# Kernel optimization log

Hardware: AMD Instinct MI355X
Metric: run time of the kernel (lower is better)

Reference implementation:

```python
import jax, jax.numpy as jnp
import numpy as np

T = 8          # num_timesteps
H = 8          # num_heads
D = 128        # lifting_dim
ROPE_BASE = 10000.0


def apply_time_only_rope(x, num_nodes, num_timesteps, base=ROPE_BASE):
    # x: [B, H, num_nodes*num_timesteps, d_head], time-major flattening
    B, Hh, S, dh = x.shape
    half = dh // 2
    times = jnp.arange(num_timesteps, dtype=jnp.float32)
    freqs = 1.0 / base ** (2.0 * jnp.arange(half, dtype=jnp.float32) / dh)
    angle = times[:, None] * freqs[None, :]                 # [T, half]
    positions = jnp.repeat(jnp.arange(num_timesteps), num_nodes)  # [S]
    cos_g = jnp.cos(angle)[positions]                       # [S, half]
    sin_g = jnp.sin(angle)[positions]
    t1 = x[..., 0::2]
    t2 = x[..., 1::2]
    r0 = t1 * cos_g - t2 * sin_g
    r1 = t1 * sin_g + t2 * cos_g
    return jnp.stack([r0, r1], axis=-1).reshape(x.shape)


def setup_inputs() -> dict:
    key = jax.random.key(0)
    ks = jax.random.split(key, 16)
    B_T, N, E = 32, 2048, 8192
    inp = {
        'x_0': jax.random.normal(ks[0], (B_T, N, D), jnp.float32),
        'edge_attr': jax.random.normal(ks[1], (B_T, E, D), jnp.float32),
        'q_data': jax.random.normal(ks[2], (B_T, N, D), jnp.float32),
    }
    def lin(k):
        kw, kb = jax.random.split(k)
        return (jax.random.normal(kw, (D, D), jnp.float32) * 0.02,
                jax.random.normal(kb, (D,), jnp.float32) * 0.02)
    inp['Wq'], inp['bq'] = lin(ks[3])
    inp['Wk0'], inp['bk0'] = lin(ks[4])
    inp['Wv0'], inp['bv0'] = lin(ks[5])
    inp['Wk1'], inp['bk1'] = lin(ks[6])
    inp['Wv1'], inp['bv1'] = lin(ks[7])
    inp['Wo'], inp['bo'] = lin(ks[8])
    return inp


def reference(x_0, edge_attr, q_data, Wq, bq, Wk0, bk0, Wv0, bv0, Wk1, bk1, Wv1, bv1, Wo, bo):
    B_T, N, d = x_0.shape
    B = B_T // T
    dh = d // H

    def flatten_st(a):  # [B*T, M, d] -> [B, T*M, d]
        return a.reshape(B, T * a.shape[1], d)

    qf = flatten_st(q_data) @ Wq.T + bq                     # [B, T*N, d]
    q = qf.reshape(B, H, N * T, dh)                         # faithful torch .view
    q = jax.nn.softmax(q, axis=-1)
    q = apply_time_only_rope(q, N, T)

    out = q
    for (feat, Wk, bk, Wv, bv) in ((x_0, Wk0, bk0, Wv0, bv0),
                                   (edge_attr, Wk1, bk1, Wv1, bv1)):
        M = feat.shape[1]
        hf = flatten_st(feat)                               # [B, T*M, d]
        k = (hf @ Wk.T + bk).reshape(B, H, M * T, dh)
        v = (hf @ Wv.T + bv).reshape(B, H, M * T, dh)
        k = apply_time_only_rope(k, M, T)
        k = jax.nn.softmax(k, axis=-1)
        k_cumsum = k.sum(axis=-2, keepdims=True)            # [B,H,1,dh]
        D_inv = 1.0 / jnp.maximum((q * k_cumsum).sum(axis=-1, keepdims=True), 1e-8)
        kv = jnp.einsum('bhsd,bhse->bhde', k, v)            # [B,H,dh,dh]
        out = q + jnp.einsum('bhsd,bhde->bhse', q, kv) * D_inv

    out = out.transpose(0, 2, 1, 3).reshape(B, N * T, d)
    out = out @ Wo.T + bo
    return out.reshape(B * T, N, d)                         # unflatten_spatiotemporal
```

## Files before the change

### kernel.cpp

```cpp
#include <hip/hip_runtime.h>
#include <hip/hip_bf16.h>
#include <math.h>


typedef __attribute__((ext_vector_type(8))) short short8;
typedef __attribute__((ext_vector_type(4))) float float4v;

#define LN1E4_OVER8 1.1512925464970229f

#define OFF_QWS   0
#define OFF_FRG_Q 4194304
#define OFF_FRG_O 4202496
#define OFF_BFRG  4210688
#define OFF_KV    4227072
#define OFF_KCS   4235264
#define OFF_PART  4235776

__device__ __forceinline__ unsigned short f2bf(float f) {
    __hip_bfloat16 h = __float2bfloat16(f);
    return *reinterpret_cast<unsigned short*>(&h);
}
__device__ __forceinline__ float bf2f(unsigned short s) {
    return __uint_as_float(((unsigned)s) << 16);
}
__device__ __forceinline__ unsigned pk2(float a, float b) {
    __hip_bfloat162 h = __float22bfloat162_rn(make_float2(a, b));
    return *reinterpret_cast<unsigned*>(&h);
}
template<int C> __device__ __forceinline__ float dppadd(float x) {
    int r = __builtin_amdgcn_update_dpp(0, __float_as_int(x), C, 0xF, 0xF, true);
    return x + __int_as_float(r);
}
__device__ __forceinline__ float sum16(float x) {
    x = dppadd<0xB1>(x);
    x = dppadd<0x4E>(x);
    x = dppadd<0x141>(x);
    x = dppadd<0x140>(x);
    return x;
}
__device__ __forceinline__ float qperm1(float x) {
    int r = __builtin_amdgcn_update_dpp(0, __float_as_int(x), 0xB1, 0xF, 0xF, true);
    return __int_as_float(r);
}

__global__ void k_prep(const float* __restrict__ Wq, const float* __restrict__ Wk1,
                       const float* __restrict__ Wv1, const float* __restrict__ Wo,
                       float* __restrict__ ws) {
    int i = blockIdx.x * 256 + threadIdx.x;
    if (i < 32768) {
        int j = i & 16383;
        int jE = j & 7, lane = (j >> 3) & 63, km = (j >> 9) & 3, cg = j >> 11;
        int n = cg * 16 + (lane & 15);
        int kk = km * 32 + (lane >> 4) * 8 + jE;
        const float* W = (i < 16384) ? Wq : Wo;
        unsigned short* dst = (unsigned short*)(ws + ((i < 16384) ? OFF_FRG_Q : OFF_FRG_O));
        dst[j] = f2bf(W[n * 128 + kk]);
    } else {
        int j = i - 32768;
        int jE = j & 7, lane = (j >> 3) & 63, km = (j >> 9) & 3, cg = j >> 11;
        int n = cg * 16 + (lane & 15);
        int k = km * 32 + (lane >> 4) * 8 + jE;
        float w = (cg < 8) ? Wk1[n * 128 + k] : Wv1[(n - 128) * 128 + k];
        ((unsigned short*)(ws + OFF_BFRG))[j] = f2bf(w);
    }
}

__global__ __launch_bounds__(256, 2) void k_q(const float* __restrict__ qd,
                                              const float* __restrict__ bq,
                                              float* __restrict__ ws) {
    __shared__ __align__(16) unsigned short aT[128 * 128];
    unsigned* qws32 = (unsigned*)(ws + OFF_QWS);
    int t = threadIdx.x, blk = blockIdx.x;
    int wave = t >> 6, lane = t & 63, quad = lane >> 4, n = lane & 15;
    long base = (long)blk * 128;
    int b = blk >> 7;
    int h = (blk & 127) >> 4;
    int s0 = (blk & 15) * 1024;
    int t1 = (blk & 15) >> 1;

    const short8* fq = (const short8*)((const unsigned short*)(ws + OFF_FRG_Q));
    short8 Bf[2][4];
    #pragma unroll
    for (int ct = 0; ct < 2; ++ct)
        #pragma unroll
        for (int km = 0; km < 4; ++km)
            Bf[ct][km] = fq[((2 * wave + ct) * 4 + km) * 64 + lane];

    #pragma unroll
    for (int i = 0; i < 16; ++i) {
        int idx = i * 256 + t;
        int row = idx >> 5, c4 = idx & 31;
        float4 v = ((const float4*)qd)[(base + row) * 32 + c4];
        unsigned short* p = aT + row * 128 + (((c4 >> 1) ^ (row & 7)) << 3) + (c4 & 1) * 4;
        *(uint2*)p = make_uint2(pk2(v.x, v.y), pk2(v.z, v.w));
    }
    __syncthreads();

    float4v acc[8][2];
    #pragma unroll
    for (int rt = 0; rt < 8; ++rt)
        #pragma unroll
        for (int ct = 0; ct < 2; ++ct) acc[rt][ct] = (float4v){0.f, 0.f, 0.f, 0.f};

    #pragma unroll
    for (int rt = 0; rt < 8; ++rt) {
        int row = rt * 16 + n;
        #pragma unroll
        for (int km = 0; km < 4; ++km) {
            short8 Af = *(const short8*)(aT + row * 128 + (((km * 4 + quad) ^ (n & 7)) << 3));
            acc[rt][0] = __builtin_amdgcn_mfma_f32_16x16x32_bf16(Af, Bf[0][km], acc[rt][0], 0, 0, 0);
            acc[rt][1] = __builtin_amdgcn_mfma_f32_16x16x32_bf16(Af, Bf[1][km], acc[rt][1], 0, 0, 0);
        }
    }

    float fr = __expf(-LN1E4_OVER8 * (float)(n >> 1));
    float sa, ca; __sincosf((float)t1 * fr, &sa, &ca);
    float sgn = (n & 1) ? sa : -sa;

    #pragma unroll
    for (int rt = 0; rt < 8; ++rt)
        #pragma unroll
        for (int ct = 0; ct < 2; ++ct) {
            int cg = 2 * wave + ct;
            float bias = bq[cg * 16 + n];
            float4v x = acc[rt][ct];
            #pragma unroll
            for (int i = 0; i < 4; ++i) {
                float e = __expf(x[i] + bias);
                float s = sum16(e);
                float q = e / s;
                float r = fmaf(qperm1(q), sgn, q * ca);
                unsigned pkd = ((unsigned)f2bf(qperm1(r)) << 16) | (unsigned)f2bf(r);
                if ((n & 1) == 0) {
                    int sp = s0 + (rt * 16 + quad * 4 + i) * 8 + cg;
                    long qoff = ((long)(b * 8 + h) * 16384 + sp) * 16 + n;
                    qws32[qoff >> 1] = pkd;
                }
            }
        }
}

__global__ __launch_bounds__(256, 3) void k_kv(const float* __restrict__ ea,
                                               const float* __restrict__ bk,
                                               const float* __restrict__ bv,
                                               float* __restrict__ ws) {
    __shared__ __align__(16) char smem[49152];
    unsigned short* aT = (unsigned short*)smem;

    int t = threadIdx.x, blk = blockIdx.x;
    int wave = t >> 6, lane = t & 63, quad = lane >> 4, n = lane & 15;
    unsigned short* kbuf = (unsigned short*)(smem + 32768) + wave * 2048;
    unsigned short* vbuf = kbuf + 1024;
    long base = (long)blk * 128;
    int sl = (blk & 511) << 7;
    int t2 = (sl & 8191) >> 10;

    #pragma unroll
    for (int i = 0; i < 16; ++i) {
        int idx = i * 256 + t;
        int row = idx >> 5, c4 = idx & 31;
        float4 v = ((const float4*)ea)[(base + row) * 32 + c4];
        unsigned short* p = aT + row * 128 + (((c4 >> 1) ^ (row & 7)) << 3) + (c4 & 1) * 4;
        *(uint2*)p = make_uint2(pk2(v.x, v.y), pk2(v.z, v.w));
    }

    const short8* bfrag = (const short8*)((const unsigned short*)(ws + OFF_BFRG));
    short8 Bf[4][4];
    #pragma unroll
    for (int ct = 0; ct < 4; ++ct) {
        int cg = (ct < 2) ? (2 * wave + ct) : (8 + 2 * wave + (ct - 2));
        #pragma unroll
        for (int km = 0; km < 4; ++km)
            Bf[ct][km] = bfrag[(cg * 4 + km) * 64 + lane];
    }

    float bias[4];
    #pragma unroll
    for (int ct = 0; ct < 4; ++ct)
        bias[ct] = (ct < 2) ? bk[(2 * wave + ct) * 16 + n] : bv[(2 * wave + ct - 2) * 16 + n];
    float fr = __expf(-LN1E4_OVER8 * (float)(n >> 1));
    float sv, cvv; __sincosf((float)t2 * fr, &sv, &cvv);
    float sgn = (n & 1) ? sv : -sv;
    float kcsacc = 0.f;
    float4v kvacc = (float4v){0.f, 0.f, 0.f, 0.f};

    __syncthreads();

    #pragma unroll
    for (int pair = 0; pair < 4; ++pair) {
        float4v acc[2][4];
        #pragma unroll
        for (int rtl = 0; rtl < 2; ++rtl)
            #pragma unroll
            for (int ct = 0; ct < 4; ++ct) acc[rtl][ct] = (float4v){0.f, 0.f, 0.f, 0.f};

        #pragma unroll
        for (int rtl = 0; rtl < 2; ++rtl) {
            int row = (pair * 2 + rtl) * 16 + n;
            short8 Af[4];
            #pragma unroll
            for (int km = 0; km < 4; ++km)
                Af[km] = *(const short8*)(aT + row * 128 + (((km * 4 + quad) ^ (n & 7)) << 3));
            #pragma unroll
            for (int ct = 0; ct < 4; ++ct)
                #pragma unroll
                for (int km = 0; km < 4; ++km)
                    acc[rtl][ct] = __builtin_amdgcn_mfma_f32_16x16x32_bf16(Af[km], Bf[ct][km], acc[rtl][ct], 0, 0, 0);
        }

        #pragma unroll
        for (int rtl = 0; rtl < 2; ++rtl)
            #pragma unroll
            for (int ct = 0; ct < 4; ++ct) {
                float x0 = acc[rtl][ct][0] + bias[ct];
                float x1 = acc[rtl][ct][1] + bias[ct];
                float x2 = acc[rtl][ct][2] + bias[ct];
                float x3 = acc[rtl][ct][3] + bias[ct];
                if (ct < 2) {
                    float p0 = __shfl_xor(x0, 1), p1 = __shfl_xor(x1, 1);
                    float p2 = __shfl_xor(x2, 1), p3 = __shfl_xor(x3, 1);
                    x0 = fmaf(p0, sgn, x0 * cvv); x1 = fmaf(p1, sgn, x1 * cvv);
                    x2 = fmaf(p2, sgn, x2 * cvv); x3 = fmaf(p3, sgn, x3 * cvv);
                    x0 = __expf(x0); x1 = __expf(x1); x2 = __expf(x2); x3 = __expf(x3);
                    float s0 = x0, s1 = x1, s2 = x2, s3 = x3;
                    s0 += __shfl_xor(s0, 1); s0 += __shfl_xor(s0, 2); s0 += __shfl_xor(s0, 4); s0 += __shfl_xor(s0, 8);
                    s1 += __shfl_xor(s1, 1); s1 += __shfl_xor(s1, 2); s1 += __shfl_xor(s1, 4); s1 += __shfl_xor(s1, 8);
                    s2 += __shfl_xor(s2, 1); s2 += __shfl_xor(s2, 2); s2 += __shfl_xor(s2, 4); s2 += __shfl_xor(s2, 8);
                    s3 += __shfl_xor(s3, 1); s3 += __shfl_xor(s3, 2); s3 += __shfl_xor(s3, 4); s3 += __shfl_xor(s3, 8);
                    x0 /= s0; x1 /= s1; x2 /= s2; x3 /= s3;
                    kcsacc += x0 + x1 + x2 + x3;
                }
                unsigned short* dst = (ct < 2) ? kbuf : vbuf;
                int o = (ct & 1) * 32 + rtl * 16 + quad * 4;
                *(uint2*)(dst + n * 64 + (((o >> 3) ^ (n & 7)) << 3) + (o & 7)) =
                    make_uint2(pk2(x0, x1), pk2(x2, x3));
            }

        asm volatile("s_waitcnt lgkmcnt(0)" ::: "memory");
        __builtin_amdgcn_sched_barrier(0);

        #pragma unroll
        for (int m = 0; m < 2; ++m) {
            int o = m * 32 + quad * 8;
            int off = (((o >> 3) ^ (n & 7)) << 3);
            short8 Ak = *(const short8*)(kbuf + n * 64 + off);
            short8 Bv = *(const short8*)(vbuf + n * 64 + off);
            kvacc = __builtin_amdgcn_mfma_f32_16x16x32_bf16(Ak, Bv, kvacc, 0, 0, 0);
        }
    }

    kcsacc += __shfl_xor(kcsacc, 16); kcsacc += __shfl_xor(kcsacc, 32);
    float* part = ws + OFF_PART + ((long)blk * 4 + wave) * 272;
    #pragma unroll
    for (int r = 0; r < 4; ++r) part[(quad * 4 + r) * 16 + n] = kvacc[r];
    if (lane < 16) part[256 + n] = kcsacc;
}

__global__ void k_red(float* __restrict__ ws) {
    int bh = blockIdx.x, t = threadIdx.x;
    if (t >= 272) return;
    const float* part = ws + OFF_PART + (long)bh * 256 * 272 + t;
    float s = 0.f;
    #pragma unroll 8
    for (int i = 0; i < 256; ++i) s += part[(long)i * 272];
    if (t < 256) ws[OFF_KV + bh * 256 + t] = s;
    else         ws[OFF_KCS + bh * 16 + (t - 256)] = s;
}

__global__ __launch_bounds__(256, 2) void k_out(const float* __restrict__ bo,
                                                float* __restrict__ ws,
                                                float* __restrict__ out) {
    __shared__ __align__(16) unsigned short tile[128 * 128];
    const unsigned short* qws16 = (const unsigned short*)(ws + OFF_QWS);
    int t = threadIdx.x, blk = blockIdx.x;
    int wave = t >> 6, lane = t & 63, quad = lane >> 4, n = lane & 15;
    int b = blk >> 7;
    int sp0 = (blk & 127) * 128;

    #pragma unroll
    for (int i = 0; i < 16; ++i) {
        int idx = i * 256 + t;
        int h = idx >> 9, rr = (idx >> 2) & 127, seg = idx & 3;
        uint2 u = *(const uint2*)(qws16 + ((long)(b * 8 + h) * 16384 + sp0 + rr) * 16 + seg * 4);
        unsigned short* p = tile + rr * 128 + (((h * 2 + (seg >> 1)) ^ (rr & 7)) << 3) + (seg & 1) * 4;
        *(uint2*)p = u;
    }

    short8 Bkv[2], Bden[2];
    #pragma unroll
    for (int ct = 0; ct < 2; ++ct) {
        int h = 2 * wave + ct;
        const float* kvp = ws + OFF_KV + (b * 8 + h) * 256;
        const float* ksp = ws + OFF_KCS + (b * 8 + h) * 16;
        short8 bk8 = {0, 0, 0, 0, 0, 0, 0, 0}, bd8 = {0, 0, 0, 0, 0, 0, 0, 0};
        bool act = (ct == 0) ? (quad < 2) : (quad >= 2);
        int kbase = (ct == 0) ? quad * 8 : (quad - 2) * 8;
        if (act) {
            #pragma unroll
            for (int jj = 0; jj < 8; ++jj) {
                bk8[jj] = (short)f2bf(kvp[(kbase + jj) * 16 + n]);
                bd8[jj] = (short)f2bf(ksp[kbase + jj]);
            }
        }
        Bkv[ct] = bk8; Bden[ct] = bd8;
    }
    const short8* fo = (const short8*)((const unsigned short*)(ws + OFF_FRG_O));
    short8 Bo[2][4];
    #pragma unroll
    for (int ct = 0; ct < 2; ++ct)
        #pragma unroll
        for (int km = 0; km < 4; ++km)
            Bo[ct][km] = fo[((2 * wave + ct) * 4 + km) * 64 + lane];
    __syncthreads();

    #pragma unroll
    for (int pass = 0; pass < 2; ++pass) {
        unsigned short fh[4][2][4];
        #pragma unroll
        for (int rtl = 0; rtl < 4; ++rtl) {
            int rt = pass * 4 + rtl;
            int row = rt * 16 + n;
            short8 Af = *(const short8*)(tile + row * 128 + (((wave * 4 + quad) ^ (n & 7)) << 3));
            float4v P0 = __builtin_amdgcn_mfma_f32_16x16x32_bf16(Af, Bkv[0], (float4v){0.f,0.f,0.f,0.f}, 0, 0, 0);
            float4v P1 = __builtin_amdgcn_mfma_f32_16x16x32_bf16(Af, Bkv[1], (float4v){0.f,0.f,0.f,0.f}, 0, 0, 0);
            float4v D0 = __builtin_amdgcn_mfma_f32_16x16x32_bf16(Af, Bden[0], (float4v){0.f,0.f,0.f,0.f}, 0, 0, 0);
            float4v D1 = __builtin_amdgcn_mfma_f32_16x16x32_bf16(Af, Bden[1], (float4v){0.f,0.f,0.f,0.f}, 0, 0, 0);
            #pragma unroll
            for (int ct = 0; ct < 2; ++ct) {
                int cg = 2 * wave + ct;
                float4v P = ct ? P1 : P0;
                float4v D = ct ? D1 : D0;
                #pragma unroll
                for (int i = 0; i < 4; ++i) {
                    int rw = rt * 16 + quad * 4 + i;
                    int col = cg * 16 + n;
                    float qv = bf2f(tile[rw * 128 + (((col >> 3) ^ (rw & 7)) << 3) + (col & 7)]);
                    float inv = 1.0f / fmaxf(D[i], 1e-8f);
                    fh[rtl][ct][i] = f2bf(fmaf(P[i], inv, qv));
                }
            }
        }
        __syncthreads();
        #pragma unroll
        for (int rtl = 0; rtl < 4; ++rtl)
            #pragma unroll
            for (int ct = 0; ct < 2; ++ct) {
                int cg = 2 * wave + ct;
                #pragma unroll
                for (int i = 0; i < 4; ++i) {
                    int rw = (pass * 4 + rtl) * 16 + quad * 4 + i;
                    int col = cg * 16 + n;
                    tile[rw * 128 + (((col >> 3) ^ (rw & 7)) << 3) + (col & 7)] = fh[rtl][ct][i];
                }
            }
    }
    __syncthreads();

    float4v acc[8][2];
    #pragma unroll
    for (int rt = 0; rt < 8; ++rt)
        #pragma unroll
        for (int ct = 0; ct < 2; ++ct) acc[rt][ct] = (float4v){0.f, 0.f, 0.f, 0.f};
    #pragma unroll
    for (int rt = 0; rt < 8; ++rt) {
        int row = rt * 16 + n;
        #pragma unroll
        for (int km = 0; km < 4; ++km) {
            short8 Af = *(const short8*)(tile + row * 128 + (((km * 4 + quad) ^ (n & 7)) << 3));
            acc[rt][0] = __builtin_amdgcn_mfma_f32_16x16x32_bf16(Af, Bo[0][km], acc[rt][0], 0, 0, 0);
            acc[rt][1] = __builtin_amdgcn_mfma_f32_16x16x32_bf16(Af, Bo[1][km], acc[rt][1], 0, 0, 0);
        }
    }
    #pragma unroll
    for (int rt = 0; rt < 8; ++rt)
        #pragma unroll
        for (int ct = 0; ct < 2; ++ct) {
            int cg = 2 * wave + ct;
            float bb = bo[cg * 16 + n];
            #pragma unroll
            for (int i = 0; i < 4; ++i) {
                float v = acc[rt][ct][i] + bb;
                float pv = qperm1(v);
                if ((n & 1) == 0) {
                    long rg = (long)b * 16384 + sp0 + rt * 16 + quad * 4 + i;
                    *(float2*)(out + rg * 128 + cg * 16 + n) = make_float2(v, pv);
                }
            }
        }
}

extern "C" void kernel_launch(void* const* d_in, const int* in_sizes, int n_in,
                              void* d_out, int out_size, void* d_ws, size_t ws_size,
                              hipStream_t stream) {
    (void)in_sizes; (void)n_in; (void)out_size; (void)ws_size;
    const float* edge = (const float*)d_in[1];
    const float* qd   = (const float*)d_in[2];
    const float* Wq   = (const float*)d_in[3];
    const float* bq   = (const float*)d_in[4];
    const float* Wk1  = (const float*)d_in[9];
    const float* bk1  = (const float*)d_in[10];
    const float* Wv1  = (const float*)d_in[11];
    const float* bv1  = (const float*)d_in[12];
    const float* Wo   = (const float*)d_in[13];
    const float* bo   = (const float*)d_in[14];
    float* ws  = (float*)d_ws;
    float* out = (float*)d_out;

    hipLaunchKernelGGL(k_prep, dim3(256),  dim3(256), 0, stream, Wq, Wk1, Wv1, Wo, ws);
    hipLaunchKernelGGL(k_q,    dim3(512),  dim3(256), 0, stream, qd, bq, ws);
    hipLaunchKernelGGL(k_kv,   dim3(2048), dim3(256), 0, stream, edge, bk1, bv1, ws);
    hipLaunchKernelGGL(k_red,  dim3(32),   dim3(320), 0, stream, ws);
    hipLaunchKernelGGL(k_out,  dim3(512),  dim3(256), 0, stream, bo, ws, out);
}
```

Baseline: 315.9 us.

## Raise occupancy in q/kv/out kernels and parallelize KV reduction with atomics

Fuses the GEMM and epilogue per row tile in k_q and k_out so only two accumulators stay live, which allows higher launch bounds. k_kv processes one 16-row tile per iteration with smaller per-wave LDS staging buffers (less shared memory) and wraps its MFMA block in s_setprio. The permute now uses DPP, and the row sums use sum16. k_red is split across 8x more blocks that atomically add into KV buffers, which k_prep now zeroes. The atomics make the float summation order nondeterministic.

```diff
diff --git a/kernel.cpp b/kernel.cpp
--- a/kernel.cpp
+++ b/kernel.cpp
@@ -55,17 +55,20 @@
         const float* W = (i < 16384) ? Wq : Wo;
         unsigned short* dst = (unsigned short*)(ws + ((i < 16384) ? OFF_FRG_Q : OFF_FRG_O));
         dst[j] = f2bf(W[n * 128 + kk]);
-    } else {
+    } else if (i < 65536) {
         int j = i - 32768;
         int jE = j & 7, lane = (j >> 3) & 63, km = (j >> 9) & 3, cg = j >> 11;
         int n = cg * 16 + (lane & 15);
         int k = km * 32 + (lane >> 4) * 8 + jE;
         float w = (cg < 8) ? Wk1[n * 128 + k] : Wv1[(n - 128) * 128 + k];
         ((unsigned short*)(ws + OFF_BFRG))[j] = f2bf(w);
-    }
-}
-
-__global__ __launch_bounds__(256, 2) void k_q(const float* __restrict__ qd,
+    } else {
+        int j = i - 65536;
+        if (j < 8704) ws[OFF_KV + j] = 0.f;
+    }
+}
+
+__global__ __launch_bounds__(256, 4) void k_q(const float* __restrict__ qd,
                                               const float* __restrict__ bq,
                                               float* __restrict__ ws) {
     __shared__ __align__(16) unsigned short aT[128 * 128];
@@ -96,34 +99,28 @@
     }
     __syncthreads();
 
-    float4v acc[8][2];
-    #pragma unroll
-    for (int rt = 0; rt < 8; ++rt)
-        #pragma unroll
-        for (int ct = 0; ct < 2; ++ct) acc[rt][ct] = (float4v){0.f, 0.f, 0.f, 0.f};
-
-    #pragma unroll
-    for (int rt = 0; rt < 8; ++rt) {
-        int row = rt * 16 + n;
-        #pragma unroll
-        for (int km = 0; km < 4; ++km) {
-            short8 Af = *(const short8*)(aT + row * 128 + (((km * 4 + quad) ^ (n & 7)) << 3));
-            acc[rt][0] = __builtin_amdgcn_mfma_f32_16x16x32_bf16(Af, Bf[0][km], acc[rt][0], 0, 0, 0);
-            acc[rt][1] = __builtin_amdgcn_mfma_f32_16x16x32_bf16(Af, Bf[1][km], acc[rt][1], 0, 0, 0);
-        }
-    }
-
     float fr = __expf(-LN1E4_OVER8 * (float)(n >> 1));
     float sa, ca; __sincosf((float)t1 * fr, &sa, &ca);
     float sgn = (n & 1) ? sa : -sa;
-
-    #pragma unroll
-    for (int rt = 0; rt < 8; ++rt)
+    float bias0 = bq[(2 * wave) * 16 + n];
+    float bias1 = bq[(2 * wave + 1) * 16 + n];
+
+    #pragma unroll
+    for (int rt = 0; rt < 8; ++rt) {
+        float4v a0 = (float4v){0.f, 0.f, 0.f, 0.f};
+        float4v a1 = (float4v){0.f, 0.f, 0.f, 0.f};
+        int row = rt * 16 + n;
+        #pragma unroll
+        for (int km = 0; km < 4; ++km) {
+            short8 Af = *(const short8*)(aT + row * 128 + (((km * 4 + quad) ^ (n & 7)) << 3));
+            a0 = __builtin_amdgcn_mfma_f32_16x16x32_bf16(Af, Bf[0][km], a0, 0, 0, 0);
+            a1 = __builtin_amdgcn_mfma_f32_16x16x32_bf16(Af, Bf[1][km], a1, 0, 0, 0);
+        }
         #pragma unroll
         for (int ct = 0; ct < 2; ++ct) {
             int cg = 2 * wave + ct;
-            float bias = bq[cg * 16 + n];
-            float4v x = acc[rt][ct];
+            float bias = ct ? bias1 : bias0;
+            float4v x = ct ? a1 : a0;
             #pragma unroll
             for (int i = 0; i < 4; ++i) {
                 float e = __expf(x[i] + bias);
@@ -138,19 +135,20 @@
                 }
             }
         }
-}
-
-__global__ __launch_bounds__(256, 3) void k_kv(const float* __restrict__ ea,
+    }
+}
+
+__global__ __launch_bounds__(256, 4) void k_kv(const float* __restrict__ ea,
                                                const float* __restrict__ bk,
                                                const float* __restrict__ bv,
                                                float* __restrict__ ws) {
-    __shared__ __align__(16) char smem[49152];
+    __shared__ __align__(16) char smem[40960];
     unsigned short* aT = (unsigned short*)smem;
 
     int t = threadIdx.x, blk = blockIdx.x;
     int wave = t >> 6, lane = t & 63, quad = lane >> 4, n = lane & 15;
-    unsigned short* kbuf = (unsigned short*)(smem + 32768) + wave * 2048;
-    unsigned short* vbuf = kbuf + 1024;
+    unsigned short* kbuf = (unsigned short*)(smem + 32768) + wave * 1024;
+    unsigned short* vbuf = kbuf + 512;
     long base = (long)blk * 128;
     int sl = (blk & 511) << 7;
     int t2 = (sl & 8191) >> 10;
@@ -187,64 +185,51 @@
     __syncthreads();
 
     #pragma unroll
-    for (int pair = 0; pair < 4; ++pair) {
-        float4v acc[2][4];
-        #pragma unroll
-        for (int rtl = 0; rtl < 2; ++rtl)
-            #pragma unroll
-            for (int ct = 0; ct < 4; ++ct) acc[rtl][ct] = (float4v){0.f, 0.f, 0.f, 0.f};
-
-        #pragma unroll
-        for (int rtl = 0; rtl < 2; ++rtl) {
-            int row = (pair * 2 + rtl) * 16 + n;
-            short8 Af[4];
+    for (int rt = 0; rt < 8; ++rt) {
+        float4v acc[4];
+        #pragma unroll
+        for (int ct = 0; ct < 4; ++ct) acc[ct] = (float4v){0.f, 0.f, 0.f, 0.f};
+
+        int row = rt * 16 + n;
+        short8 Af[4];
+        #pragma unroll
+        for (int km = 0; km < 4; ++km)
+            Af[km] = *(const short8*)(aT + row * 128 + (((km * 4 + quad) ^ (n & 7)) << 3));
+        __builtin_amdgcn_s_setprio(1);
+        #pragma unroll
+        for (int ct = 0; ct < 4; ++ct)
             #pragma unroll
             for (int km = 0; km < 4; ++km)
-                Af[km] = *(const short8*)(aT + row * 128 + (((km * 4 + quad) ^ (n & 7)) << 3));
-            #pragma unroll
-            for (int ct = 0; ct < 4; ++ct)
-                #pragma unroll
-                for (int km = 0; km < 4; ++km)
-                    acc[rtl][ct] = __builtin_amdgcn_mfma_f32_16x16x32_bf16(Af[km], Bf[ct][km], acc[rtl][ct], 0, 0, 0);
-        }
-
-        #pragma unroll
-        for (int rtl = 0; rtl < 2; ++rtl)
-            #pragma unroll
-            for (int ct = 0; ct < 4; ++ct) {
-                float x0 = acc[rtl][ct][0] + bias[ct];
-                float x1 = acc[rtl][ct][1] + bias[ct];
-                float x2 = acc[rtl][ct][2] + bias[ct];
-                float x3 = acc[rtl][ct][3] + bias[ct];
-                if (ct < 2) {
-                    float p0 = __shfl_xor(x0, 1), p1 = __shfl_xor(x1, 1);
-                    float p2 = __shfl_xor(x2, 1), p3 = __shfl_xor(x3, 1);
-                    x0 = fmaf(p0, sgn, x0 * cvv); x1 = fmaf(p1, sgn, x1 * cvv);
-                    x2 = fmaf(p2, sgn, x2 * cvv); x3 = fmaf(p3, sgn, x3 * cvv);
-                    x0 = __expf(x0); x1 = __expf(x1); x2 = __expf(x2); x3 = __expf(x3);
-                    float s0 = x0, s1 = x1, s2 = x2, s3 = x3;
-                    s0 += __shfl_xor(s0, 1); s0 += __shfl_xor(s0, 2); s0 += __shfl_xor(s0, 4); s0 += __shfl_xor(s0, 8);
-                    s1 += __shfl_xor(s1, 1); s1 += __shfl_xor(s1, 2); s1 += __shfl_xor(s1, 4); s1 += __shfl_xor(s1, 8);
-                    s2 += __shfl_xor(s2, 1); s2 += __shfl_xor(s2, 2); s2 += __shfl_xor(s2, 4); s2 += __shfl_xor(s2, 8);
-                    s3 += __shfl_xor(s3, 1); s3 += __shfl_xor(s3, 2); s3 += __shfl_xor(s3, 4); s3 += __shfl_xor(s3, 8);
-                    x0 /= s0; x1 /= s1; x2 /= s2; x3 /= s3;
-                    kcsacc += x0 + x1 + x2 + x3;
-                }
-                unsigned short* dst = (ct < 2) ? kbuf : vbuf;
-                int o = (ct & 1) * 32 + rtl * 16 + quad * 4;
-                *(uint2*)(dst + n * 64 + (((o >> 3) ^ (n & 7)) << 3) + (o & 7)) =
-                    make_uint2(pk2(x0, x1), pk2(x2, x3));
-            }
+                acc[ct] = __builtin_amdgcn_mfma_f32_16x16x32_bf16(Af[km], Bf[ct][km], acc[ct], 0, 0, 0);
+        __builtin_amdgcn_s_setprio(0);
+
+        #pragma unroll
+        for (int ct = 0; ct < 4; ++ct) {
+            float x0 = acc[ct][0] + bias[ct];
+            float x1 = acc[ct][1] + bias[ct];
+            float x2 = acc[ct][2] + bias[ct];
+            float x3 = acc[ct][3] + bias[ct];
+            if (ct < 2) {
+                x0 = fmaf(qperm1(x0), sgn, x0 * cvv); x1 = fmaf(qperm1(x1), sgn, x1 * cvv);
+                x2 = fmaf(qperm1(x2), sgn, x2 * cvv); x3 = fmaf(qperm1(x3), sgn, x3 * cvv);
+                x0 = __expf(x0); x1 = __expf(x1); x2 = __expf(x2); x3 = __expf(x3);
+                float s0 = sum16(x0), s1 = sum16(x1), s2 = sum16(x2), s3 = sum16(x3);
+                x0 /= s0; x1 /= s1; x2 /= s2; x3 /= s3;
+                kcsacc += x0 + x1 + x2 + x3;
+            }
+            unsigned short* dst = (ct < 2) ? kbuf : vbuf;
+            int o = (ct & 1) * 16 + quad * 4;
+            *(uint2*)(dst + n * 32 + (((o >> 3) ^ (n & 3)) << 3) + (o & 7)) =
+                make_uint2(pk2(x0, x1), pk2(x2, x3));
+        }
 
         asm volatile("s_waitcnt lgkmcnt(0)" ::: "memory");
         __builtin_amdgcn_sched_barrier(0);
 
-        #pragma unroll
-        for (int m = 0; m < 2; ++m) {
-            int o = m * 32 + quad * 8;
-            int off = (((o >> 3) ^ (n & 7)) << 3);
-            short8 Ak = *(const short8*)(kbuf + n * 64 + off);
-            short8 Bv = *(const short8*)(vbuf + n * 64 + off);
+        {
+            int off = ((quad ^ (n & 3)) << 3);
+            short8 Ak = *(const short8*)(kbuf + n * 32 + off);
+            short8 Bv = *(const short8*)(vbuf + n * 32 + off);
             kvacc = __builtin_amdgcn_mfma_f32_16x16x32_bf16(Ak, Bv, kvacc, 0, 0, 0);
         }
     }
@@ -257,17 +242,19 @@
 }
 
 __global__ void k_red(float* __restrict__ ws) {
-    int bh = blockIdx.x, t = threadIdx.x;
+    int blk = blockIdx.x, t = threadIdx.x;
     if (t >= 272) return;
-    const float* part = ws + OFF_PART + (long)bh * 256 * 272 + t;
+    int bh = blk >> 3, g = blk & 7;
+    const float* part = ws + OFF_PART + (long)bh * 256 * 272 + (long)g * 32 * 272 + t;
     float s = 0.f;
     #pragma unroll 8
-    for (int i = 0; i < 256; ++i) s += part[(long)i * 272];
-    if (t < 256) ws[OFF_KV + bh * 256 + t] = s;
-    else         ws[OFF_KCS + bh * 16 + (t - 256)] = s;
-}
-
-__global__ __launch_bounds__(256, 2) void k_out(const float* __restrict__ bo,
+    for (int i = 0; i < 32; ++i) s += part[(long)i * 272];
+    float* dst = (t < 256) ? (ws + OFF_KV + bh * 256 + t)
+                           : (ws + OFF_KCS + bh * 16 + (t - 256));
+    atomicAdd(dst, s);
+}
+
+__global__ __launch_bounds__(256, 3) void k_out(const float* __restrict__ bo,
                                                 float* __restrict__ ws,
                                                 float* __restrict__ out) {
     __shared__ __align__(16) unsigned short tile[128 * 128];
@@ -356,30 +343,27 @@
     }
     __syncthreads();
 
-    float4v acc[8][2];
-    #pragma unroll
-    for (int rt = 0; rt < 8; ++rt)
-        #pragma unroll
-        for (int ct = 0; ct < 2; ++ct) acc[rt][ct] = (float4v){0.f, 0.f, 0.f, 0.f};
+    float bb0 = bo[(2 * wave) * 16 + n];
+    float bb1 = bo[(2 * wave + 1) * 16 + n];
     #pragma unroll
     for (int rt = 0; rt < 8; ++rt) {
+        float4v a0 = (float4v){0.f, 0.f, 0.f, 0.f};
+        float4v a1 = (float4v){0.f, 0.f, 0.f, 0.f};
         int row = rt * 16 + n;
         #pragma unroll
         for (int km = 0; km < 4; ++km) {
             short8 Af = *(const short8*)(tile + row * 128 + (((km * 4 + quad) ^ (n & 7)) << 3));
-            acc[rt][0] = __builtin_amdgcn_mfma_f32_16x16x32_bf16(Af, Bo[0][km], acc[rt][0], 0, 0, 0);
-            acc[rt][1] = __builtin_amdgcn_mfma_f32_16x16x32_bf16(Af, Bo[1][km], acc[rt][1], 0, 0, 0);
-        }
-    }
-    #pragma unroll
-    for (int rt = 0; rt < 8; ++rt)
+            a0 = __builtin_amdgcn_mfma_f32_16x16x32_bf16(Af, Bo[0][km], a0, 0, 0, 0);
+            a1 = __builtin_amdgcn_mfma_f32_16x16x32_bf16(Af, Bo[1][km], a1, 0, 0, 0);
+        }
         #pragma unroll
         for (int ct = 0; ct < 2; ++ct) {
             int cg = 2 * wave + ct;
-            float bb = bo[cg * 16 + n];
+            float bb = ct ? bb1 : bb0;
+            float4v a = ct ? a1 : a0;
             #pragma unroll
             for (int i = 0; i < 4; ++i) {
-                float v = acc[rt][ct][i] + bb;
+                float v = a[i] + bb;
                 float pv = qperm1(v);
                 if ((n & 1) == 0) {
                     long rg = (long)b * 16384 + sp0 + rt * 16 + quad * 4 + i;
@@ -387,6 +371,7 @@
                 }
             }
         }
+    }
 }
 
 extern "C" void kernel_launch(void* const* d_in, const int* in_sizes, int n_in,
@@ -406,9 +391,9 @@
     float* ws  = (float*)d_ws;
     float* out = (float*)d_out;
 
-    hipLaunchKernelGGL(k_prep, dim3(256),  dim3(256), 0, stream, Wq, Wk1, Wv1, Wo, ws);
+    hipLaunchKernelGGL(k_prep, dim3(290),  dim3(256), 0, stream, Wq, Wk1, Wv1, Wo, ws);
     hipLaunchKernelGGL(k_q,    dim3(512),  dim3(256), 0, stream, qd, bq, ws);
     hipLaunchKernelGGL(k_kv,   dim3(2048), dim3(256), 0, stream, edge, bk1, bv1, ws);
-    hipLaunchKernelGGL(k_red,  dim3(32),   dim3(320), 0, stream, ws);
+    hipLaunchKernelGGL(k_red,  dim3(256),  dim3(320), 0, stream, ws);
     hipLaunchKernelGGL(k_out,  dim3(512),  dim3(256), 0, stream, bo, ws, out);
 }
```

After: 298.9 us. 5.4% less time.
